# Optimization experiments

Measured on AMD Instinct MI355X. Metric: run time of the kernel, lower is better.

Reference implementation:

```python
import jax, jax.numpy as jnp
import numpy as np

N_NODES = 50000


def gcn_conv(x, src, dst, W, b, n_nodes):
    # PyG GCNConv: add self-loops, symmetric normalization D^-1/2 (A+I) D^-1/2 (x W) + b
    E = src.shape[0]
    deg = jax.ops.segment_sum(jnp.ones((E,), x.dtype), dst, num_segments=n_nodes) + 1.0
    dinv = jax.lax.rsqrt(deg)
    h = x @ W  # [N, H]
    norm = dinv[src] * dinv[dst]  # [E]
    agg = jax.ops.segment_sum(h[src] * norm[:, None], dst, num_segments=n_nodes)
    agg = agg + h * (dinv * dinv)[:, None]  # self-loop contribution
    return agg + b


def setup_inputs() -> dict:
    key = jax.random.key(0)
    ks = jax.random.split(key, 16)
    N, E, D, H, T, O = N_NODES, 800000, 128, 128, 2, 1
    x = jax.random.normal(ks[0], (N, D), jnp.float32)
    edge_index = jax.random.randint(ks[1], (2, E), 0, N, jnp.int32)
    edge_attrs = jax.random.uniform(ks[2], (T, E, 7), jnp.float32)
    s = lambda k, sh: jax.random.normal(k, sh, jnp.float32) * (1.0 / np.sqrt(sh[0]))
    return {
        "x": x, "edge_index": edge_index, "edge_attrs": edge_attrs,
        "W1": s(ks[3], (D, H)), "b1": jnp.zeros((H,), jnp.float32),
        "W2": s(ks[4], (H, H)), "b2": jnp.zeros((H,), jnp.float32),
        "W3": s(ks[5], (H, H)), "b3": jnp.zeros((H,), jnp.float32),
        "We": s(ks[6], (2 * H + 7, H)), "be": jnp.zeros((H,), jnp.float32),
        "Wg": s(ks[7], (H, O)), "bg": jnp.zeros((O,), jnp.float32),
    }


def reference(x, edge_index, edge_attrs, W1, b1, W2, b2, W3, b3, We, be, Wg, bg):
    src, dst = edge_index[0], edge_index[1]
    n = x.shape[0]
    outputs = []
    for t in range(edge_attrs.shape[0]):  # small fixed T, x evolves across iterations
        edge_attr = edge_attrs[t]
        x = jax.nn.relu(gcn_conv(x, src, dst, W1, b1, n))
        x = jax.nn.relu(gcn_conv(x, src, dst, W2, b2, n))
        x = jax.nn.relu(gcn_conv(x, src, dst, W3, b3, n))
        # gather-concat-MLP-mean per edge
        edge_features = jnp.concatenate([x[src], x[dst], edge_attr], axis=1)
        edge_output = jax.nn.relu(edge_features @ We + be)
        graph_features = jnp.mean(edge_output, axis=0, keepdims=True)  # [1, H]
        outputs.append(graph_features @ Wg + bg)
        W1 = W2  # no-op placeholder removed below
        W1 = W1  # keep W1 unchanged
    return jnp.concatenate(outputs, axis=0)  # [T, output_dim]
```

## Files before the change

kernel.cpp:

```cpp
#include <hip/hip_runtime.h>
#include <hip/hip_bf16.h>


typedef __attribute__((ext_vector_type(8))) short bf16x8;
typedef __attribute__((ext_vector_type(4))) float f32x4;
typedef __attribute__((ext_vector_type(2))) float f32x2;

__device__ __forceinline__ unsigned short f2bf(float f) {
    union { float f; unsigned int u; } v; v.f = f;
    unsigned int r = v.u + 0x7fffu + ((v.u >> 16) & 1u);
    return (unsigned short)(r >> 16);
}
__device__ __forceinline__ unsigned int pk2bf(float lo, float hi) {
    return (unsigned int)f2bf(lo) | ((unsigned int)f2bf(hi) << 16);
}
__device__ __forceinline__ unsigned char f2fp8(float f) {
    return (unsigned char)(__builtin_amdgcn_cvt_pk_fp8_f32(f, f, 0, false) & 0xff);
}
__device__ __forceinline__ void fp8x4(unsigned int u, float* o) {
    f32x2 lo = __builtin_amdgcn_cvt_pk_f32_fp8(u, false);
    f32x2 hi = __builtin_amdgcn_cvt_pk_f32_fp8(u, true);
    o[0] = lo[0]; o[1] = lo[1]; o[2] = hi[0]; o[3] = hi[1];
}
__device__ __forceinline__ void de16add(uint4 v, float* a) {
    float t[4];
    fp8x4(v.x, t); a[0]+=t[0]; a[1]+=t[1]; a[2]+=t[2]; a[3]+=t[3];
    fp8x4(v.y, t); a[4]+=t[0]; a[5]+=t[1]; a[6]+=t[2]; a[7]+=t[3];
    fp8x4(v.z, t); a[8]+=t[0]; a[9]+=t[1]; a[10]+=t[2]; a[11]+=t[3];
    fp8x4(v.w, t); a[12]+=t[0]; a[13]+=t[1]; a[14]+=t[2]; a[15]+=t[3];
}

__global__ void to_bf16(const float* __restrict__ in, unsigned short* __restrict__ out, int n4)
{
    int i = blockIdx.x * 256 + threadIdx.x;
    if (i < n4) {
        float4 v = ((const float4*)in)[i];
        ushort4 o;
        o.x = f2bf(v.x); o.y = f2bf(v.y); o.z = f2bf(v.z); o.w = f2bf(v.w);
        ((ushort4*)out)[i] = o;
    }
}

__global__ void transpose_w(
    const float* __restrict__ W1, const float* __restrict__ W2,
    const float* __restrict__ W3, const float* __restrict__ We,
    unsigned short* __restrict__ T1, unsigned short* __restrict__ T2,
    unsigned short* __restrict__ T3, unsigned short* __restrict__ Tuv)
{
    const float* src; unsigned short* dst;
    switch (blockIdx.y) {
        case 0:  src = W1;             dst = T1;               break;
        case 1:  src = W2;             dst = T2;               break;
        case 2:  src = W3;             dst = T3;               break;
        case 3:  src = We;             dst = Tuv;              break;
        case 4:  src = We + 128 * 128; dst = Tuv + 128 * 128;  break;
        default: src = W2;             dst = Tuv + 256 * 128;  break;
    }
    for (int i = blockIdx.x * 256 + threadIdx.x; i < 128 * 128; i += 256 * gridDim.x) {
        int k = i >> 7, c = i & 127;
        dst[c * 128 + k] = f2bf(src[i]);
    }
}

__global__ __launch_bounds__(256) void mfma_matmul(
    const unsigned short* __restrict__ X, const unsigned short* __restrict__ Wt,
    unsigned char* __restrict__ out, const float* __restrict__ scale, int n_rows)
{
    const int wave = threadIdx.x >> 6;
    const int lane = threadIdx.x & 63;
    const int m = lane & 15;
    const int q = lane >> 4;
    const int r = blockIdx.x * 64 + wave * 16 + m;
    const bool rv = r < n_rows;

    f32x4 acc[8];
    #pragma unroll
    for (int i = 0; i < 8; ++i) acc[i] = (f32x4){0.f, 0.f, 0.f, 0.f};

    #pragma unroll
    for (int k0 = 0; k0 < 128; k0 += 32) {
        bf16x8 a = {};
        if (rv) a = *(const bf16x8*)(X + (size_t)r * 128 + k0 + q * 8);
        #pragma unroll
        for (int ct = 0; ct < 8; ++ct) {
            bf16x8 b = *(const bf16x8*)(Wt + (ct * 16 + m) * 128 + k0 + q * 8);
            acc[ct] = __builtin_amdgcn_mfma_f32_16x16x32_bf16(a, b, acc[ct], 0, 0, 0);
        }
    }

    #pragma unroll
    for (int reg = 0; reg < 4; ++reg) {
        int gr = blockIdx.x * 64 + wave * 16 + q * 4 + reg;
        if (gr >= n_rows) continue;
        float s = scale[gr];
        #pragma unroll
        for (int ct = 0; ct < 8; ++ct)
            out[(size_t)gr * 128 + ct * 16 + m] = f2fp8(acc[ct][reg] * s);
    }
}

#define FPAD 136
__global__ __launch_bounds__(256) void fused_gm(
    const unsigned char* __restrict__ hs_in, const int* __restrict__ csr_src,
    const int* __restrict__ offs, const int* __restrict__ counts,
    const float* __restrict__ dinv, const float* __restrict__ bias,
    const unsigned short* __restrict__ Wt, int ncols, int uvcols,
    unsigned char* __restrict__ buv, unsigned char* __restrict__ bh, int n)
{
    __shared__ unsigned short xs[64 * FPAD];
    const int tid = threadIdx.x;

    #pragma unroll
    for (int half = 0; half < 2; ++half) {
        int row  = half * 32 + (tid >> 3);
        int node = blockIdx.x * 64 + row;
        if (node < n) {
            int c16 = (tid & 7) * 16;
            int off = offs[node];
            int cnt = counts[node];

            float a[16] = {};
            de16add(*(const uint4*)(hs_in + (size_t)node * 128 + c16), a);
            int j = 0;
            for (; j + 4 <= cnt; j += 4) {
                int s0 = csr_src[off + j + 0];
                int s1 = csr_src[off + j + 1];
                int s2 = csr_src[off + j + 2];
                int s3 = csr_src[off + j + 3];
                uint4 h0 = *(const uint4*)(hs_in + (size_t)s0 * 128 + c16);
                uint4 h1 = *(const uint4*)(hs_in + (size_t)s1 * 128 + c16);
                uint4 h2 = *(const uint4*)(hs_in + (size_t)s2 * 128 + c16);
                uint4 h3 = *(const uint4*)(hs_in + (size_t)s3 * 128 + c16);
                de16add(h0, a); de16add(h1, a); de16add(h2, a); de16add(h3, a);
            }
            for (; j < cnt; ++j) {
                int s = csr_src[off + j];
                de16add(*(const uint4*)(hs_in + (size_t)s * 128 + c16), a);
            }

            float dn = dinv[node];
            #pragma unroll
            for (int i = 0; i < 4; ++i) {
                float4 bb = *(const float4*)(bias + c16 + i * 4);
                float r0 = fmaxf(fmaf(a[i*4+0], dn, bb.x), 0.f);
                float r1 = fmaxf(fmaf(a[i*4+1], dn, bb.y), 0.f);
                float r2 = fmaxf(fmaf(a[i*4+2], dn, bb.z), 0.f);
                float r3 = fmaxf(fmaf(a[i*4+3], dn, bb.w), 0.f);
                *(unsigned int*)&xs[row * FPAD + c16 + i*4 + 0] = pk2bf(r0, r1);
                *(unsigned int*)&xs[row * FPAD + c16 + i*4 + 2] = pk2bf(r2, r3);
            }
        }
    }
    __syncthreads();

    const int wave = tid >> 6;
    const int lane = tid & 63;
    const int m = lane & 15;
    const int q = lane >> 4;
    const int nct = ncols >> 4;

    for (int ct = 0; ct < nct; ++ct) {
        f32x4 acc = (f32x4){0.f, 0.f, 0.f, 0.f};
        #pragma unroll
        for (int k0 = 0; k0 < 128; k0 += 32) {
            bf16x8 a = *(const bf16x8*)&xs[(wave * 16 + m) * FPAD + k0 + q * 8];
            bf16x8 b = *(const bf16x8*)(Wt + (size_t)(ct * 16 + m) * 128 + k0 + q * 8);
            acc = __builtin_amdgcn_mfma_f32_16x16x32_bf16(a, b, acc, 0, 0, 0);
        }
        int col = ct * 16 + m;
        #pragma unroll
        for (int reg = 0; reg < 4; ++reg) {
            int node = blockIdx.x * 64 + wave * 16 + q * 4 + reg;
            if (node >= n) continue;
            if (col < uvcols)
                buv[(size_t)node * 256 + col] = f2fp8(acc[reg]);
            else
                bh[(size_t)node * 128 + col - uvcols] = f2fp8(acc[reg] * dinv[node]);
        }
    }
}

#define EM_CHUNK 256
__global__ __launch_bounds__(256) void edge_mlp(
    const unsigned char* __restrict__ uv, const int* __restrict__ src,
    const int* __restrict__ dst, const float* __restrict__ ea,
    const float* __restrict__ We_e, const float* __restrict__ be,
    const float* __restrict__ Wg, float* __restrict__ acc, int E)
{
    const int tid  = threadIdx.x;
    const int lane = tid & 31;
    const int g    = tid >> 5;
    const int c4   = lane * 4;

    __shared__ float eas[EM_CHUNK * 7];
    __shared__ int   ss[EM_CHUNK];
    __shared__ int   ds[EM_CHUNK];
    __shared__ float red[256];

    float4 w[7];
    #pragma unroll
    for (int i = 0; i < 7; ++i)
        w[i] = *(const float4*)(We_e + i * 128 + c4);
    const float4 be4 = *(const float4*)(be + c4);
    const float4 wg4 = *(const float4*)(Wg + c4);

    float4 part = make_float4(0.f, 0.f, 0.f, 0.f);

    for (int base = blockIdx.x * EM_CHUNK; base < E; base += gridDim.x * EM_CHUNK) {
        const int nch = min(EM_CHUNK, E - base);
        for (int i = tid; i < nch * 7; i += 256)
            eas[i] = ea[(size_t)base * 7 + i];
        for (int i = tid; i < nch; i += 256) {
            ss[i] = src[base + i];
            ds[i] = dst[base + i];
        }
        __syncthreads();

        auto ev = [&](int j) {
            unsigned int us = *(const unsigned int*)(uv + (size_t)ss[j] * 256 + c4);
            unsigned int vs = *(const unsigned int*)(uv + (size_t)ds[j] * 256 + 128 + c4);
            float uf[4], vf[4];
            fp8x4(us, uf); fp8x4(vs, vf);
            const float* eav = &eas[j * 7];
            float4 val;
            val.x = uf[0] + vf[0] + be4.x;
            val.y = uf[1] + vf[1] + be4.y;
            val.z = uf[2] + vf[2] + be4.z;
            val.w = uf[3] + vf[3] + be4.w;
            #pragma unroll
            for (int i = 0; i < 7; ++i) {
                float e = eav[i];
                val.x = fmaf(e, w[i].x, val.x);
                val.y = fmaf(e, w[i].y, val.y);
                val.z = fmaf(e, w[i].z, val.z);
                val.w = fmaf(e, w[i].w, val.w);
            }
            part.x += fmaxf(val.x, 0.f);
            part.y += fmaxf(val.y, 0.f);
            part.z += fmaxf(val.z, 0.f);
            part.w += fmaxf(val.w, 0.f);
        };

        int j = g;
        for (; j + 32 <= nch; j += 32) {
            ev(j); ev(j + 8); ev(j + 16); ev(j + 24);
        }
        for (; j < nch; j += 8)
            ev(j);
        __syncthreads();
    }

    float p = part.x * wg4.x + part.y * wg4.y + part.z * wg4.z + part.w * wg4.w;
    red[tid] = p;
    __syncthreads();
    for (int s = 128; s > 0; s >>= 1) {
        if (tid < s) red[tid] += red[tid + s];
        __syncthreads();
    }
    if (tid == 0) atomicAdd(acc, red[0]);
}

__global__ void count_edges(const int* __restrict__ dst, int* __restrict__ counts, int E)
{
    int e = blockIdx.x * 256 + threadIdx.x;
    if (e < E) atomicAdd(&counts[dst[e]], 1);
}

__global__ void compute_dinv(const int* __restrict__ counts, float* __restrict__ dinv, int n)
{
    int i = blockIdx.x * 256 + threadIdx.x;
    if (i < n) dinv[i] = rsqrtf((float)counts[i] + 1.0f);
}

__global__ void scan1(const int* __restrict__ counts, int* __restrict__ scanned,
                      int* __restrict__ btot, int n)
{
    __shared__ int sh[256];
    int i = blockIdx.x * 256 + threadIdx.x;
    int v = (i < n) ? counts[i] : 0;
    sh[threadIdx.x] = v;
    __syncthreads();
    for (int off = 1; off < 256; off <<= 1) {
        int t = (threadIdx.x >= off) ? sh[threadIdx.x - off] : 0;
        __syncthreads();
        sh[threadIdx.x] += t;
        __syncthreads();
    }
    if (i < n) scanned[i] = sh[threadIdx.x] - v;
    if (threadIdx.x == 255) btot[blockIdx.x] = sh[255];
}

__global__ void scan2(int* __restrict__ btot, int nb)
{
    __shared__ int sh[256];
    int v = (threadIdx.x < nb) ? btot[threadIdx.x] : 0;
    sh[threadIdx.x] = v;
    __syncthreads();
    for (int off = 1; off < 256; off <<= 1) {
        int t = (threadIdx.x >= off) ? sh[threadIdx.x - off] : 0;
        __syncthreads();
        sh[threadIdx.x] += t;
        __syncthreads();
    }
    if (threadIdx.x < nb) btot[threadIdx.x] = sh[threadIdx.x] - v;
}

__global__ void scan3(const int* __restrict__ scanned, const int* __restrict__ btot,
                      int* __restrict__ offs, int* __restrict__ cursor, int n)
{
    int i = blockIdx.x * 256 + threadIdx.x;
    if (i < n) {
        int o = scanned[i] + btot[blockIdx.x];
        offs[i] = o;
        cursor[i] = o;
    }
}

__global__ void fill_csr(const int* __restrict__ src, const int* __restrict__ dst,
                         int* __restrict__ cursor, int* __restrict__ csr_src, int E)
{
    int e = blockIdx.x * 256 + threadIdx.x;
    if (e < E) {
        int slot = atomicAdd(&cursor[dst[e]], 1);
        csr_src[slot] = src[e];
    }
}

__global__ void write_out(const float* __restrict__ acc, const float* __restrict__ bg,
                          float* __restrict__ out, float invE, int T)
{
    int t = threadIdx.x;
    if (t < T) out[t] = acc[t] * invE + bg[0];
}


extern "C" void kernel_launch(void* const* d_in, const int* in_sizes, int n_in,
                              void* d_out, int out_size, void* d_ws, size_t ws_size,
                              hipStream_t stream)
{
    const float* x   = (const float*)d_in[0];
    const int*  eidx = (const int*)d_in[1];
    const float* ea  = (const float*)d_in[2];
    const float* W1  = (const float*)d_in[3];
    const float* b1  = (const float*)d_in[4];
    const float* W2  = (const float*)d_in[5];
    const float* b2  = (const float*)d_in[6];
    const float* W3  = (const float*)d_in[7];
    const float* b3  = (const float*)d_in[8];
    const float* We  = (const float*)d_in[9];
    const float* be  = (const float*)d_in[10];
    const float* Wg  = (const float*)d_in[11];
    const float* bg  = (const float*)d_in[12];

    const int N = in_sizes[0] / 128;
    const int E = in_sizes[1] / 2;
    const int T = in_sizes[2] / (E * 7);
    const int* src = eidx;
    const int* dst = eidx + E;

    char* wsp = (char*)d_ws;
    auto alloc = [&](size_t bytes) -> char* {
        char* p = wsp;
        wsp += (bytes + 255) / 256 * 256;
        return p;
    };
    int*   counts  = (int*)alloc((size_t)N * 4);
    int*   offs    = (int*)alloc((size_t)N * 4);
    int*   cursor  = (int*)alloc((size_t)N * 4);
    int*   scanned = (int*)alloc((size_t)N * 4);
    int*   btot    = (int*)alloc(1024);
    int*   csr_src = (int*)alloc((size_t)E * 4);
    float* dinv    = (float*)alloc((size_t)N * 4);
    float* acc     = (float*)alloc(256);
    unsigned short* X0  = (unsigned short*)alloc((size_t)N * 128 * 2);
    unsigned char*  Bh0 = (unsigned char*)alloc((size_t)N * 128);
    unsigned char*  Bh1 = (unsigned char*)alloc((size_t)N * 128);
    unsigned char*  Buv = (unsigned char*)alloc((size_t)N * 256);
    unsigned short* T1  = (unsigned short*)alloc(128 * 128 * 2);
    unsigned short* T2  = (unsigned short*)alloc(128 * 128 * 2);
    unsigned short* T3  = (unsigned short*)alloc(128 * 128 * 2);
    unsigned short* Tuv = (unsigned short*)alloc(384 * 128 * 2);

    hipMemsetAsync(counts, 0, (size_t)N * 4, stream);
    hipMemsetAsync(acc, 0, (size_t)T * 4, stream);

    to_bf16<<<(N * 128 / 4 + 255) / 256, 256, 0, stream>>>(x, X0, N * 128 / 4);
    transpose_w<<<dim3(8, 6), 256, 0, stream>>>(W1, W2, W3, We, T1, T2, T3, Tuv);

    count_edges<<<(E + 255) / 256, 256, 0, stream>>>(dst, counts, E);
    compute_dinv<<<(N + 255) / 256, 256, 0, stream>>>(counts, dinv, N);
    const int nb = (N + 255) / 256;
    scan1<<<nb, 256, 0, stream>>>(counts, scanned, btot, N);
    scan2<<<1, 256, 0, stream>>>(btot, nb);
    scan3<<<nb, 256, 0, stream>>>(scanned, btot, offs, cursor, N);
    fill_csr<<<(E + 255) / 256, 256, 0, stream>>>(src, dst, cursor, csr_src, E);

    const int mmb = (N + 63) / 64;
    const int emb = (E + EM_CHUNK - 1) / EM_CHUNK;

    unsigned char* hcur = Bh0;
    unsigned char* hnxt = Bh1;

    for (int t = 0; t < T; ++t) {
        if (t == 0) {
            mfma_matmul<<<mmb, 256, 0, stream>>>(X0, T1, hcur, dinv, N);
        }
        fused_gm<<<mmb, 256, 0, stream>>>(hcur, csr_src, offs, counts, dinv, b1,
                                          T2, 128, 0, Buv, hnxt, N);
        { unsigned char* tmp = hcur; hcur = hnxt; hnxt = tmp; }
        fused_gm<<<mmb, 256, 0, stream>>>(hcur, csr_src, offs, counts, dinv, b2,
                                          T3, 128, 0, Buv, hnxt, N);
        { unsigned char* tmp = hcur; hcur = hnxt; hnxt = tmp; }
        bool last = (t == T - 1);
        fused_gm<<<mmb, 256, 0, stream>>>(hcur, csr_src, offs, counts, dinv, b3,
                                          Tuv, last ? 256 : 384, 256, Buv, hnxt, N);
        if (!last) { unsigned char* tmp = hcur; hcur = hnxt; hnxt = tmp; }

        edge_mlp<<<emb, 256, 0, stream>>>(Buv, src, dst, ea + (size_t)t * E * 7,
                                          We + 256 * 128, be, Wg, acc + t, E);
    }
    write_out<<<1, 64, 0, stream>>>(acc, bg, (float*)d_out, 1.0f / (float)E, T);
}
```

Measured before the change: 613.5 us.

## Shrink fused GCN block to 32 nodes and software-pipeline neighbor gathers

The fused aggregate+matmul kernel now handles 32 nodes per block instead of 64. Each thread owns one node row slice instead of two sequential halves, which doubles the block count and gives more parallelism across the memory-latency-bound gather. The neighbor loop is restructured to prefetch the next 8 neighbor rows while accumulating the previous 8, keeping more loads in flight. The MFMA stage splits column tiles across wave pairs so all four waves stay busy. The cost is more registers per thread, which may lower occupancy.

```diff
diff --git a/kernel.cpp b/kernel.cpp
--- a/kernel.cpp
+++ b/kernel.cpp
@@ -100,6 +100,7 @@
 }
 
 #define FPAD 136
+#define GN 32
 __global__ __launch_bounds__(256) void fused_gm(
     const unsigned char* __restrict__ hs_in, const int* __restrict__ csr_src,
     const int* __restrict__ offs, const int* __restrict__ counts,
@@ -107,48 +108,60 @@
     const unsigned short* __restrict__ Wt, int ncols, int uvcols,
     unsigned char* __restrict__ buv, unsigned char* __restrict__ bh, int n)
 {
-    __shared__ unsigned short xs[64 * FPAD];
+    __shared__ unsigned short xs[GN * FPAD];
     const int tid = threadIdx.x;
-
-    #pragma unroll
-    for (int half = 0; half < 2; ++half) {
-        int row  = half * 32 + (tid >> 3);
-        int node = blockIdx.x * 64 + row;
-        if (node < n) {
-            int c16 = (tid & 7) * 16;
-            int off = offs[node];
-            int cnt = counts[node];
-
-            float a[16] = {};
-            de16add(*(const uint4*)(hs_in + (size_t)node * 128 + c16), a);
-            int j = 0;
-            for (; j + 4 <= cnt; j += 4) {
-                int s0 = csr_src[off + j + 0];
-                int s1 = csr_src[off + j + 1];
-                int s2 = csr_src[off + j + 2];
-                int s3 = csr_src[off + j + 3];
-                uint4 h0 = *(const uint4*)(hs_in + (size_t)s0 * 128 + c16);
-                uint4 h1 = *(const uint4*)(hs_in + (size_t)s1 * 128 + c16);
-                uint4 h2 = *(const uint4*)(hs_in + (size_t)s2 * 128 + c16);
-                uint4 h3 = *(const uint4*)(hs_in + (size_t)s3 * 128 + c16);
-                de16add(h0, a); de16add(h1, a); de16add(h2, a); de16add(h3, a);
+    const int row = tid >> 3;
+    const int node = blockIdx.x * GN + row;
+    const int c16 = (tid & 7) * 16;
+
+    if (node < n) {
+        const int off = offs[node];
+        const int cnt = counts[node];
+
+        float a[16] = {};
+        de16add(*(const uint4*)(hs_in + (size_t)node * 128 + c16), a);
+
+        int j = 0;
+        if (cnt >= 8) {
+            int i0[8];
+            #pragma unroll
+            for (int q = 0; q < 8; ++q) i0[q] = csr_src[off + q];
+            uint4 h0[8];
+            #pragma unroll
+            for (int q = 0; q < 8; ++q)
+                h0[q] = *(const uint4*)(hs_in + (size_t)i0[q] * 128 + c16);
+            j = 8;
+            for (; j + 8 <= cnt; j += 8) {
+                int i1[8];
+                #pragma unroll
+                for (int q = 0; q < 8; ++q) i1[q] = csr_src[off + j + q];
+                uint4 h1[8];
+                #pragma unroll
+                for (int q = 0; q < 8; ++q)
+                    h1[q] = *(const uint4*)(hs_in + (size_t)i1[q] * 128 + c16);
+                #pragma unroll
+                for (int q = 0; q < 8; ++q) de16add(h0[q], a);
+                #pragma unroll
+                for (int q = 0; q < 8; ++q) h0[q] = h1[q];
             }
-            for (; j < cnt; ++j) {
-                int s = csr_src[off + j];
-                de16add(*(const uint4*)(hs_in + (size_t)s * 128 + c16), a);
-            }
-
-            float dn = dinv[node];
             #pragma unroll
-            for (int i = 0; i < 4; ++i) {
-                float4 bb = *(const float4*)(bias + c16 + i * 4);
-                float r0 = fmaxf(fmaf(a[i*4+0], dn, bb.x), 0.f);
-                float r1 = fmaxf(fmaf(a[i*4+1], dn, bb.y), 0.f);
-                float r2 = fmaxf(fmaf(a[i*4+2], dn, bb.z), 0.f);
-                float r3 = fmaxf(fmaf(a[i*4+3], dn, bb.w), 0.f);
-                *(unsigned int*)&xs[row * FPAD + c16 + i*4 + 0] = pk2bf(r0, r1);
-                *(unsigned int*)&xs[row * FPAD + c16 + i*4 + 2] = pk2bf(r2, r3);
-            }
+            for (int q = 0; q < 8; ++q) de16add(h0[q], a);
+        }
+        for (; j < cnt; ++j) {
+            int s = csr_src[off + j];
+            de16add(*(const uint4*)(hs_in + (size_t)s * 128 + c16), a);
+        }
+
+        float dn = dinv[node];
+        #pragma unroll
+        for (int i = 0; i < 4; ++i) {
+            float4 bb = *(const float4*)(bias + c16 + i * 4);
+            float r0 = fmaxf(fmaf(a[i*4+0], dn, bb.x), 0.f);
+            float r1 = fmaxf(fmaf(a[i*4+1], dn, bb.y), 0.f);
+            float r2 = fmaxf(fmaf(a[i*4+2], dn, bb.z), 0.f);
+            float r3 = fmaxf(fmaf(a[i*4+3], dn, bb.w), 0.f);
+            *(unsigned int*)&xs[row * FPAD + c16 + i*4 + 0] = pk2bf(r0, r1);
+            *(unsigned int*)&xs[row * FPAD + c16 + i*4 + 2] = pk2bf(r2, r3);
         }
     }
     __syncthreads();
@@ -157,25 +170,29 @@
     const int lane = tid & 63;
     const int m = lane & 15;
     const int q = lane >> 4;
+    const int rt = (wave & 1) * 16;
     const int nct = ncols >> 4;
-
-    for (int ct = 0; ct < nct; ++ct) {
+    const int half = nct >> 1;
+    const int ct0 = (wave >> 1) * half;
+
+    for (int ci = 0; ci < half; ++ci) {
+        const int ct = ct0 + ci;
         f32x4 acc = (f32x4){0.f, 0.f, 0.f, 0.f};
         #pragma unroll
         for (int k0 = 0; k0 < 128; k0 += 32) {
-            bf16x8 a = *(const bf16x8*)&xs[(wave * 16 + m) * FPAD + k0 + q * 8];
+            bf16x8 a = *(const bf16x8*)&xs[(rt + m) * FPAD + k0 + q * 8];
             bf16x8 b = *(const bf16x8*)(Wt + (size_t)(ct * 16 + m) * 128 + k0 + q * 8);
             acc = __builtin_amdgcn_mfma_f32_16x16x32_bf16(a, b, acc, 0, 0, 0);
         }
-        int col = ct * 16 + m;
+        const int col = ct * 16 + m;
         #pragma unroll
         for (int reg = 0; reg < 4; ++reg) {
-            int node = blockIdx.x * 64 + wave * 16 + q * 4 + reg;
-            if (node >= n) continue;
+            int nd = blockIdx.x * GN + rt + q * 4 + reg;
+            if (nd >= n) continue;
             if (col < uvcols)
-                buv[(size_t)node * 256 + col] = f2fp8(acc[reg]);
+                buv[(size_t)nd * 256 + col] = f2fp8(acc[reg]);
             else
-                bh[(size_t)node * 128 + col - uvcols] = f2fp8(acc[reg] * dinv[node]);
+                bh[(size_t)nd * 128 + col - uvcols] = f2fp8(acc[reg] * dinv[nd]);
         }
     }
 }
@@ -396,6 +413,7 @@
     fill_csr<<<(E + 255) / 256, 256, 0, stream>>>(src, dst, cursor, csr_src, E);
 
     const int mmb = (N + 63) / 64;
+    const int fgb = (N + GN - 1) / GN;
     const int emb = (E + EM_CHUNK - 1) / EM_CHUNK;
 
     unsigned char* hcur = Bh0;
@@ -405,14 +423,14 @@
         if (t == 0) {
             mfma_matmul<<<mmb, 256, 0, stream>>>(X0, T1, hcur, dinv, N);
         }
-        fused_gm<<<mmb, 256, 0, stream>>>(hcur, csr_src, offs, counts, dinv, b1,
+        fused_gm<<<fgb, 256, 0, stream>>>(hcur, csr_src, offs, counts, dinv, b1,
                                           T2, 128, 0, Buv, hnxt, N);
         { unsigned char* tmp = hcur; hcur = hnxt; hnxt = tmp; }
-        fused_gm<<<mmb, 256, 0, stream>>>(hcur, csr_src, offs, counts, dinv, b2,
+        fused_gm<<<fgb, 256, 0, stream>>>(hcur, csr_src, offs, counts, dinv, b2,
                                           T3, 128, 0, Buv, hnxt, N);
         { unsigned char* tmp = hcur; hcur = hnxt; hnxt = tmp; }
         bool last = (t == T - 1);
-        fused_gm<<<mmb, 256, 0, stream>>>(hcur, csr_src, offs, counts, dinv, b3,
+        fused_gm<<<fgb, 256, 0, stream>>>(hcur, csr_src, offs, counts, dinv, b3,
                                           Tuv, last ? 256 : 384, 256, Buv, hnxt, N);
         if (!last) { unsigned char* tmp = hcur; hcur = hnxt; hnxt = tmp; }
 
```

After: 644.7 us. 1.05x slower.
